# Kernel optimization log

Hardware: AMD Instinct MI355X
Metric: run time of the kernel (lower is better)

Reference implementation:

```python
import jax, jax.numpy as jnp
import numpy as np

N_QUBITS = 14
STATE_DIM = 2 ** N_QUBITS  # 16384
BATCH, SEQ = 4, 2048


def setup_inputs() -> dict:
    key = jax.random.key(0)
    ks = jax.random.split(key, 5)
    x = jax.random.normal(ks[0], (BATCH, SEQ), dtype=jnp.float32)
    rotation_params = jax.random.normal(ks[1], (N_QUBITS, 3), dtype=jnp.float32)
    entangling_params = jax.random.normal(ks[2], (N_QUBITS - 1,), dtype=jnp.float32)
    # classical_encoder: Linear(1, n_qubits) -> Tanh -> Linear(n_qubits, state_dim) -> Softmax
    W1 = jax.random.normal(ks[3], (1, N_QUBITS), dtype=jnp.float32)
    b1 = jnp.zeros((N_QUBITS,), dtype=jnp.float32)
    W2 = jax.random.normal(ks[4], (N_QUBITS, STATE_DIM), dtype=jnp.float32) * 0.1
    b2 = jnp.zeros((STATE_DIM,), dtype=jnp.float32)
    return {"x": x, "rotation_params": rotation_params,
            "entangling_params": entangling_params,
            "W1": W1, "b1": b1, "W2": W2, "b2": b2}


def reference(x, rotation_params, entangling_params, W1, b1, W2, b2):
    # classical_encoder applied to each scalar x[i,j] -> softmax weights [B,S,D]
    h = jnp.tanh(x[..., None] * W1[0] + b1)          # [B,S,nq]
    w = jax.nn.softmax(h @ W2 + b2, axis=-1)         # [B,S,D]
    # Per-qubit rotation scalar factors (independent of x), multiplied together
    half = rotation_params * 0.5
    c, s = jnp.cos(half), jnp.sin(half)              # [nq,3]
    rot_factors = c[:, 0] * c[:, 1] * c[:, 2] + 1j * (s[:, 0] * s[:, 1] * s[:, 2])
    # Per-pair parameterized-CNOT scalar factors
    cs = jax.nn.sigmoid(entangling_params)
    ent_factors = cs + 1j * (1.0 - cs)
    total = (jnp.prod(rot_factors) * jnp.prod(ent_factors)).astype(jnp.complex64)
    # state starts as e0; all scalar multiplies keep only component 0 nonzero,
    # then elementwise multiply by classical weights.
    out = jnp.zeros(w.shape, dtype=jnp.complex64)
    out = out.at[..., 0].set(total * w[..., 0].astype(jnp.complex64))
    return out
```

## Files before the change

### kernel.cpp

```cpp
#include <hip/hip_runtime.h>
#include <math.h>

constexpr int NQ    = 14;
constexpr int DIM   = 16384;
constexpr int BATCH = 4;
constexpr int SEQ   = 2048;
constexpr int NPOS  = BATCH * SEQ;
constexpr int P     = 4;
constexpr int TPB   = 256;

typedef float vf4 __attribute__((ext_vector_type(4)));
typedef float vf2 __attribute__((ext_vector_type(2)));

__device__ __forceinline__ float uniform_f(float v) {
    return __int_as_float(__builtin_amdgcn_readfirstlane(__float_as_int(v)));
}


template <bool CPLX>
__global__ void __launch_bounds__(TPB)
qenc_kernel(const float* __restrict__ x,
            const float* __restrict__ rot,
            const float* __restrict__ ent,
            const float* __restrict__ W1,
            const float* __restrict__ b1,
            const float* __restrict__ W2,
            const float* __restrict__ b2,
            float* __restrict__ out)
{
    __shared__ float sh_h[P * NQ];
    __shared__ float sh_tot_re, sh_tot_im;
    __shared__ float sh_z0[P];
    __shared__ float red[4][P];

    const int tid  = threadIdx.x;
    const int wid  = tid >> 6;
    const int lane = tid & 63;
    const long long pos0 = (long long)blockIdx.x * P;

    if (tid < P * NQ) {
        const int p = tid / NQ;
        const int k = tid - p * NQ;
        sh_h[tid] = tanhf(x[pos0 + p] * W1[k] + b1[k]);
    }
    if (tid == 64) {
        float tre = 1.0f, tim = 0.0f;
        for (int q = 0; q < NQ; ++q) {
            const float a0 = 0.5f * rot[q * 3 + 0];
            const float a1 = 0.5f * rot[q * 3 + 1];
            const float a2 = 0.5f * rot[q * 3 + 2];
            const float fre = cosf(a0) * cosf(a1) * cosf(a2);
            const float fim = sinf(a0) * sinf(a1) * sinf(a2);
            const float nre = tre * fre - tim * fim;
            const float nim = tre * fim + tim * fre;
            tre = nre; tim = nim;
        }
        for (int q = 0; q < NQ - 1; ++q) {
            const float cs  = 1.0f / (1.0f + __expf(-ent[q]));
            const float nre = tre * cs - tim * (1.0f - cs);
            const float nim = tre * (1.0f - cs) + tim * cs;
            tre = nre; tim = nim;
        }
        sh_tot_re = tre; sh_tot_im = tim;
    }
    __syncthreads();

    float h[P][NQ];
#pragma unroll
    for (int p = 0; p < P; ++p)
#pragma unroll
        for (int k = 0; k < NQ; ++k)
            h[p][k] = uniform_f(sh_h[p * NQ + k]);

    float acc[P];
#pragma unroll
    for (int p = 0; p < P; ++p) acc[p] = 0.0f;

    constexpr int ITERS = DIM / (4 * TPB);
    for (int i = 0; i < ITERS; ++i) {
        const int d = 4 * (tid + TPB * i);
        float4 wv[NQ];
#pragma unroll
        for (int k = 0; k < NQ; ++k)
            wv[k] = *reinterpret_cast<const float4*>(W2 + (size_t)k * DIM + d);
        const float4 bb = *reinterpret_cast<const float4*>(b2 + d);
        const bool d0 = (d == 0);
#pragma unroll
        for (int p = 0; p < P; ++p) {
            float za = bb.x, zb = bb.y, zc = bb.z, zd = bb.w;
#pragma unroll
            for (int k = 0; k < NQ; ++k) {
                za = fmaf(h[p][k], wv[k].x, za);
                zb = fmaf(h[p][k], wv[k].y, zb);
                zc = fmaf(h[p][k], wv[k].z, zc);
                zd = fmaf(h[p][k], wv[k].w, zd);
            }
            acc[p] += (__expf(za) + __expf(zb)) + (__expf(zc) + __expf(zd));

            if constexpr (CPLX) {
                float* rowp = out + (size_t)(pos0 + p) * (2 * (size_t)DIM) + 2 * d;
                vf4 z4 = {0.f, 0.f, 0.f, 0.f};
                if (!d0) {
                    *reinterpret_cast<vf4*>(rowp)     = z4;
                    *reinterpret_cast<vf4*>(rowp + 4) = z4;
                } else {
                    sh_z0[p] = za;
                    vf2 z2 = {0.f, 0.f};
                    *reinterpret_cast<vf2*>(rowp + 2) = z2;
                    *reinterpret_cast<vf4*>(rowp + 4) = z4;
                }
            } else {
                float* rowp = out + (size_t)(pos0 + p) * (size_t)DIM + d;
                if (!d0) {
                    vf4 z4 = {0.f, 0.f, 0.f, 0.f};
                    *reinterpret_cast<vf4*>(rowp) = z4;
                } else {
                    sh_z0[p] = za;
                    rowp[1] = 0.f;
                    rowp[2] = 0.f;
                    rowp[3] = 0.f;
                }
            }
        }
    }

#pragma unroll
    for (int p = 0; p < P; ++p) {
        float v = acc[p];
#pragma unroll
        for (int off = 32; off > 0; off >>= 1)
            v += __shfl_down(v, off, 64);
        if (lane == 0) red[wid][p] = v;
    }
    __syncthreads();
    if (tid < P) {
        const float denom = (red[0][tid] + red[1][tid]) + (red[2][tid] + red[3][tid]);
        const float w0 = __expf(sh_z0[tid]) / denom;
        const size_t stride = CPLX ? 2 * (size_t)DIM : (size_t)DIM;
        float* rowp = out + (size_t)(pos0 + tid) * stride;
        rowp[0] = sh_tot_re * w0;
        if constexpr (CPLX) rowp[1] = sh_tot_im * w0;
    }
}

extern "C" void kernel_launch(void* const* d_in, const int* in_sizes, int n_in,
                              void* d_out, int out_size, void* d_ws, size_t ws_size,
                              hipStream_t stream) {
    (void)in_sizes; (void)n_in; (void)d_ws; (void)ws_size;
    const float* x   = (const float*)d_in[0];
    const float* rot = (const float*)d_in[1];
    const float* ent = (const float*)d_in[2];
    const float* W1  = (const float*)d_in[3];
    const float* b1  = (const float*)d_in[4];
    const float* W2  = (const float*)d_in[5];
    const float* b2  = (const float*)d_in[6];
    float* out = (float*)d_out;

    const long long cplx_elems = (long long)NPOS * 2LL * DIM;
    if ((long long)out_size >= cplx_elems) {
        qenc_kernel<true><<<NPOS / P, TPB, 0, stream>>>(x, rot, ent, W1, b1, W2, b2, out);
    } else {
        qenc_kernel<false><<<NPOS / P, TPB, 0, stream>>>(x, rot, ent, W1, b1, W2, b2, out);
    }
}
```

Measured before the change: 578.1 us.

## Split output zeroing into memset and widen positions per block

Zero-filling the large output moves out of the compute kernel into a hipMemsetAsync, so the kernel only computes the softmax denominator and writes element 0 per row. Positions per block rise from 4 to 16, which reuses each W2 load across more rows, and h values are now read from shared memory as vectors rather than held in registers. The z0 logit is recomputed at the end instead of being captured during the loop. In exchange there is an extra memset launch, heavier LDS traffic, and higher register pressure from 16 accumulators.

After: 635.0 us. 1.1x slower.

```diff
diff --git a/kernel.cpp b/kernel.cpp
--- a/kernel.cpp
+++ b/kernel.cpp
@@ -6,32 +6,25 @@
 constexpr int BATCH = 4;
 constexpr int SEQ   = 2048;
 constexpr int NPOS  = BATCH * SEQ;
-constexpr int P     = 4;
 constexpr int TPB   = 256;
-
-typedef float vf4 __attribute__((ext_vector_type(4)));
-typedef float vf2 __attribute__((ext_vector_type(2)));
-
-__device__ __forceinline__ float uniform_f(float v) {
-    return __int_as_float(__builtin_amdgcn_readfirstlane(__float_as_int(v)));
-}
+constexpr int P     = 16;
+constexpr int NBLK  = NPOS / P;
 
 
 template <bool CPLX>
 __global__ void __launch_bounds__(TPB)
-qenc_kernel(const float* __restrict__ x,
-            const float* __restrict__ rot,
-            const float* __restrict__ ent,
-            const float* __restrict__ W1,
-            const float* __restrict__ b1,
-            const float* __restrict__ W2,
-            const float* __restrict__ b2,
-            float* __restrict__ out)
+qenc_compute(const float* __restrict__ x,
+             const float* __restrict__ rot,
+             const float* __restrict__ ent,
+             const float* __restrict__ W1,
+             const float* __restrict__ b1,
+             const float* __restrict__ W2,
+             const float* __restrict__ b2,
+             float* __restrict__ out)
 {
-    __shared__ float sh_h[P * NQ];
+    __shared__ float sh_h[P * 16];
+    __shared__ float red[4][P];
     __shared__ float sh_tot_re, sh_tot_im;
-    __shared__ float sh_z0[P];
-    __shared__ float red[4][P];
 
     const int tid  = threadIdx.x;
     const int wid  = tid >> 6;
@@ -41,9 +34,9 @@
     if (tid < P * NQ) {
         const int p = tid / NQ;
         const int k = tid - p * NQ;
-        sh_h[tid] = tanhf(x[pos0 + p] * W1[k] + b1[k]);
+        sh_h[p * 16 + k] = tanhf(x[pos0 + p] * W1[k] + b1[k]);
     }
-    if (tid == 64) {
+    if (tid == 240) {
         float tre = 1.0f, tim = 0.0f;
         for (int q = 0; q < NQ; ++q) {
             const float a0 = 0.5f * rot[q * 3 + 0];
@@ -65,13 +58,6 @@
     }
     __syncthreads();
 
-    float h[P][NQ];
-#pragma unroll
-    for (int p = 0; p < P; ++p)
-#pragma unroll
-        for (int k = 0; k < NQ; ++k)
-            h[p][k] = uniform_f(sh_h[p * NQ + k]);
-
     float acc[P];
 #pragma unroll
     for (int p = 0; p < P; ++p) acc[p] = 0.0f;
@@ -84,43 +70,26 @@
         for (int k = 0; k < NQ; ++k)
             wv[k] = *reinterpret_cast<const float4*>(W2 + (size_t)k * DIM + d);
         const float4 bb = *reinterpret_cast<const float4*>(b2 + d);
-        const bool d0 = (d == 0);
+
 #pragma unroll
         for (int p = 0; p < P; ++p) {
+            const float4 ha = *reinterpret_cast<const float4*>(&sh_h[p * 16 + 0]);
+            const float4 hb = *reinterpret_cast<const float4*>(&sh_h[p * 16 + 4]);
+            const float4 hc = *reinterpret_cast<const float4*>(&sh_h[p * 16 + 8]);
+            const float2 he = *reinterpret_cast<const float2*>(&sh_h[p * 16 + 12]);
+            const float hh[NQ] = {ha.x, ha.y, ha.z, ha.w,
+                                  hb.x, hb.y, hb.z, hb.w,
+                                  hc.x, hc.y, hc.z, hc.w,
+                                  he.x, he.y};
             float za = bb.x, zb = bb.y, zc = bb.z, zd = bb.w;
 #pragma unroll
             for (int k = 0; k < NQ; ++k) {
-                za = fmaf(h[p][k], wv[k].x, za);
-                zb = fmaf(h[p][k], wv[k].y, zb);
-                zc = fmaf(h[p][k], wv[k].z, zc);
-                zd = fmaf(h[p][k], wv[k].w, zd);
+                za = fmaf(hh[k], wv[k].x, za);
+                zb = fmaf(hh[k], wv[k].y, zb);
+                zc = fmaf(hh[k], wv[k].z, zc);
+                zd = fmaf(hh[k], wv[k].w, zd);
             }
             acc[p] += (__expf(za) + __expf(zb)) + (__expf(zc) + __expf(zd));
-
-            if constexpr (CPLX) {
-                float* rowp = out + (size_t)(pos0 + p) * (2 * (size_t)DIM) + 2 * d;
-                vf4 z4 = {0.f, 0.f, 0.f, 0.f};
-                if (!d0) {
-                    *reinterpret_cast<vf4*>(rowp)     = z4;
-                    *reinterpret_cast<vf4*>(rowp + 4) = z4;
-                } else {
-                    sh_z0[p] = za;
-                    vf2 z2 = {0.f, 0.f};
-                    *reinterpret_cast<vf2*>(rowp + 2) = z2;
-                    *reinterpret_cast<vf4*>(rowp + 4) = z4;
-                }
-            } else {
-                float* rowp = out + (size_t)(pos0 + p) * (size_t)DIM + d;
-                if (!d0) {
-                    vf4 z4 = {0.f, 0.f, 0.f, 0.f};
-                    *reinterpret_cast<vf4*>(rowp) = z4;
-                } else {
-                    sh_z0[p] = za;
-                    rowp[1] = 0.f;
-                    rowp[2] = 0.f;
-                    rowp[3] = 0.f;
-                }
-            }
         }
     }
 
@@ -133,9 +102,14 @@
         if (lane == 0) red[wid][p] = v;
     }
     __syncthreads();
+
     if (tid < P) {
         const float denom = (red[0][tid] + red[1][tid]) + (red[2][tid] + red[3][tid]);
-        const float w0 = __expf(sh_z0[tid]) / denom;
+        float z0 = b2[0];
+#pragma unroll
+        for (int k = 0; k < NQ; ++k)
+            z0 = fmaf(sh_h[tid * 16 + k], W2[(size_t)k * DIM], z0);
+        const float w0 = __expf(z0) / denom;
         const size_t stride = CPLX ? 2 * (size_t)DIM : (size_t)DIM;
         float* rowp = out + (size_t)(pos0 + tid) * stride;
         rowp[0] = sh_tot_re * w0;
@@ -158,8 +132,10 @@
 
     const long long cplx_elems = (long long)NPOS * 2LL * DIM;
     if ((long long)out_size >= cplx_elems) {
-        qenc_kernel<true><<<NPOS / P, TPB, 0, stream>>>(x, rot, ent, W1, b1, W2, b2, out);
+        hipMemsetAsync(d_out, 0, (size_t)NPOS * 2 * (size_t)DIM * sizeof(float), stream);
+        qenc_compute<true><<<NBLK, TPB, 0, stream>>>(x, rot, ent, W1, b1, W2, b2, out);
     } else {
-        qenc_kernel<false><<<NPOS / P, TPB, 0, stream>>>(x, rot, ent, W1, b1, W2, b2, out);
+        hipMemsetAsync(d_out, 0, (size_t)NPOS * (size_t)DIM * sizeof(float), stream);
+        qenc_compute<false><<<NBLK, TPB, 0, stream>>>(x, rot, ent, W1, b1, W2, b2, out);
     }
 }
```
